# Kernel tuning notes

Measured on AMD Instinct MI355X. Metric: run time of the kernel, lower is better.

The kernel has to match this reference:

```python
import jax, jax.numpy as jnp
import numpy as np

DIM_PROBLEM = 256
DIM_CONTEXT = 1024
DIM_HIDDEN = 4096
INIT = 0.01


def setup_inputs() -> dict:
    key = jax.random.key(0)
    ks = jax.random.split(key, 12)
    H, C = DIM_HIDDEN, DIM_CONTEXT
    inp = {
        "context": jax.random.normal(ks[0], (C,), dtype=jnp.float32),
        "u": jax.random.uniform(ks[1], (DIM_PROBLEM,), dtype=jnp.float32),
        "l1_w": jax.random.normal(ks[2], (1, C), dtype=jnp.float32) * INIT,
        "l1_b": jnp.zeros((1,), dtype=jnp.float32),
        "Wf_w": jax.random.normal(ks[3], (H, H + 1), dtype=jnp.float32) * INIT,
        "Wf_b": jnp.zeros((H,), dtype=jnp.float32),
        "Wi_w": jax.random.normal(ks[4], (H, H + 1), dtype=jnp.float32) * INIT,
        "Wi_b": jnp.zeros((H,), dtype=jnp.float32),
        "Wc_w": jax.random.normal(ks[5], (H, H + 1), dtype=jnp.float32) * INIT,
        "Wc_b": jnp.zeros((H,), dtype=jnp.float32),
        "Wo_w": jax.random.normal(ks[6], (1, H + 1), dtype=jnp.float32) * INIT,
        "Wo_b": jnp.zeros((1,), dtype=jnp.float32),
    }
    return inp


def reference(context, u, l1_w, l1_b, Wf_w, Wf_b, Wi_w, Wi_b, Wc_w, Wc_b, Wo_w, Wo_b):
    H = Wf_w.shape[0]
    x0 = l1_w @ context + l1_b                      # (1,)
    h0 = jnp.zeros((H,), dtype=context.dtype)       # T.Tensor(H) treated as zeros
    c0 = jnp.zeros((H,), dtype=context.dtype)
    logp0 = jnp.zeros((1,), dtype=context.dtype)

    def step(carry, u_t):
        h, c, x, logp = carry
        z = jnp.concatenate([h, x])                 # (H+1,)
        f = jax.nn.sigmoid(Wf_w @ z + Wf_b)         # (H,)
        i = jax.nn.sigmoid(Wi_w @ z + Wi_b)
        cc = jnp.tanh(Wc_w @ z + Wc_b)
        o = jax.nn.sigmoid(Wo_w @ z + Wo_b)         # (1,)
        c_new = f * c + i * cc
        h_new = o * jnp.tanh(c_new)                 # broadcast (1,)*(H,)
        # detached Bernoulli(o) sample via pre-drawn uniform noise
        s = (u_t < jax.lax.stop_gradient(o)).astype(x.dtype)  # (1,)
        # log p accumulated: log(p * o^s * (1-o)^(1-s)) = logp + s*log o + (1-s)*log(1-o)
        logp_new = logp + s * jnp.log(o) + (1.0 - s) * jnp.log(1.0 - o)
        return (h_new, c_new, s, logp_new), s

    (_, _, _, logp), sol = jax.lax.scan(step, (h0, c0, x0, logp0), u)
    solution = sol[:, None, :]                      # (dim_problem, 1, 1)
    return solution, logp
```

## Files before the change

kernel.cpp:

```cpp
#include <hip/hip_runtime.h>
#include <hip/hip_fp16.h>
#include <stdint.h>


#define HID    4096
#define CTX    1024
#define NSTEPS 256
#define NBLK   256
#define TPB    1024
#define WAVES  16
#define HROWS  16
#define GROWS  48
#define RPW    3
#define NCH    8

typedef _Float16 h2 __attribute__((ext_vector_type(2)));

__device__ __forceinline__ float fdot2f(uint32_t a, uint32_t b, float c) {
#if __has_builtin(__builtin_amdgcn_fdot2)
  return __builtin_amdgcn_fdot2(__builtin_bit_cast(h2, a),
                                __builtin_bit_cast(h2, b), c, false);
#else
  h2 x = __builtin_bit_cast(h2, a), y = __builtin_bit_cast(h2, b);
  return c + (float)x[0]*(float)y[0] + (float)x[1]*(float)y[1];
#endif
}
__device__ __forceinline__ uint32_t pkf16(float x, float y) {
  h2 v; v[0] = (_Float16)x; v[1] = (_Float16)y;
  return __builtin_bit_cast(uint32_t, v);
}
__device__ __forceinline__ uint4 cvt8(const float* p) {
  return make_uint4(pkf16(p[0],p[1]), pkf16(p[2],p[3]),
                    pkf16(p[4],p[5]), pkf16(p[6],p[7]));
}
__device__ __forceinline__ float dot4(float acc, uint4 a, uint4 b) {
  acc = fdot2f(a.x, b.x, acc); acc = fdot2f(a.y, b.y, acc);
  acc = fdot2f(a.z, b.z, acc); acc = fdot2f(a.w, b.w, acc);
  return acc;
}
__device__ __forceinline__ void agw(uint32_t &slot, uint32_t v) {
  asm volatile("v_accvgpr_write_b32 %0, %1" : "=a"(slot) : "v"(v));
}
__device__ __forceinline__ uint32_t agr(uint32_t slot) {
  uint32_t v;
  asm("v_accvgpr_read_b32 %0, %1" : "=v"(v) : "a"(slot));
  return v;
}
__device__ __forceinline__ void stT(uint64_t* p, uint32_t payload, uint32_t tag) {
  const uint64_t v = ((uint64_t)tag << 32) | (uint64_t)payload;
  __hip_atomic_store(p, v, __ATOMIC_RELAXED, __HIP_MEMORY_SCOPE_AGENT);
}
__device__ __forceinline__ uint64_t ldT(const uint64_t* p) {
  return __hip_atomic_load(p, __ATOMIC_RELAXED, __HIP_MEMORY_SCOPE_AGENT);
}

__global__ __launch_bounds__(TPB)
void lstm(const float* __restrict__ ctx, const float* __restrict__ u,
          const float* __restrict__ l1w, const float* __restrict__ l1b,
          const float* __restrict__ Wf,  const float* __restrict__ Wfb,
          const float* __restrict__ Wi,  const float* __restrict__ Wib,
          const float* __restrict__ Wc,  const float* __restrict__ Wcb,
          const float* __restrict__ Wow, const float* __restrict__ Wob,
          uint64_t* __restrict__ hh0, uint64_t* __restrict__ hh1,
          uint64_t* __restrict__ part0, uint64_t* __restrict__ part1,
          float* __restrict__ out)
{
  __shared__ uint4 wlds[WAVES][HID/8];
  __shared__ uint4 zsh4[HID/8];
  __shared__ float red[WAVES];
  __shared__ float pre[GROWS];
  __shared__ float cst[HROWS];
  __shared__ float bias[GROWS];
  __shared__ float wx[GROWS];
  __shared__ float x0sh, osh, ssh;

  const int tid  = threadIdx.x;
  const int b    = blockIdx.x;
  const int wv   = tid >> 6;
  const int lane = tid & 63;

  uint32_t* z32 = (uint32_t*)zsh4;
  for (int i = tid; i < HID/2; i += TPB) z32[i] = 0u;
  if (tid < HROWS) cst[tid] = 0.f;
  if (tid < GROWS) {
    int g = tid / HROWS, j = tid % HROWS;
    const float* bw = (g==0 ? Wfb : (g==1 ? Wib : Wcb));
    const float* gw = (g==0 ? Wf  : (g==1 ? Wi  : Wc ));
    bias[tid] = bw[b*HROWS + j];
    wx[tid]   = gw[(size_t)(b*HROWS + j)*4097 + 4096];
  }

  const float wolocal = (tid < HROWS) ? Wow[b*HROWS + tid] : 0.f;
  const float woxw = Wow[HID];
  const float wob0 = Wob[0];

  uint32_t wreg[64];
  {
    const int fl0 = wv*RPW;
    const int g0 = (fl0+0)/HROWS, j0 = (fl0+0)%HROWS;
    const int g1 = (fl0+1)/HROWS, j1 = (fl0+1)%HROWS;
    const int g2 = (fl0+2)/HROWS, j2 = (fl0+2)%HROWS;
    const float* r0 = (g0==0?Wf:(g0==1?Wi:Wc)) + (size_t)(b*HROWS+j0)*4097;
    const float* r1 = (g1==0?Wf:(g1==1?Wi:Wc)) + (size_t)(b*HROWS+j1)*4097;
    const float* r2 = (g2==0?Wf:(g2==1?Wi:Wc)) + (size_t)(b*HROWS+j2)*4097;
    #pragma unroll
    for (int c = 0; c < NCH; ++c) {
      const int col = c*512 + lane*8;
      const uint4 va = cvt8(r0 + col);
      agw(wreg[c*8+0], va.x); agw(wreg[c*8+1], va.y);
      agw(wreg[c*8+2], va.z); agw(wreg[c*8+3], va.w);
      const uint4 vb = cvt8(r1 + col);
      agw(wreg[c*8+4], vb.x); agw(wreg[c*8+5], vb.y);
      agw(wreg[c*8+6], vb.z); agw(wreg[c*8+7], vb.w);
      wlds[wv][c*64 + lane] = cvt8(r2 + col);
    }
  }

  {
    float p = l1w[tid] * ctx[tid];
    #pragma unroll
    for (int off = 32; off; off >>= 1) p += __shfl_down(p, off, 64);
    __syncthreads();
    if (lane == 0) red[wv] = p;
    __syncthreads();
    if (tid == 0) {
      float ssum = 0.f;
      for (int w = 0; w < WAVES; ++w) ssum += red[w];
      x0sh = ssum + l1b[0];
    }
    __syncthreads();
  }
  float xcur = x0sh;
  float logp = 0.f;
  float ut = u[0];

  for (int t = 0; t < NSTEPS; ++t) {
    const uint64_t* prd = (t & 1) ? part0 : part1;
    uint64_t pv0 = 0, pv1 = 0, pv2 = 0, pv3 = 0;
    if (wv == 0 && t > 0) {
      pv0 = ldT(&prd[lane*4+0]); pv1 = ldT(&prd[lane*4+1]);
      pv2 = ldT(&prd[lane*4+2]); pv3 = ldT(&prd[lane*4+3]);
    }

    float a0 = 0.f, a1 = 0.f, a2 = 0.f;
    #pragma unroll
    for (int c = 0; c < NCH; ++c) {
      const uint4 zz = zsh4[c*64 + lane];
      const uint4 wl = wlds[wv][c*64 + lane];
      a0 = fdot2f(agr(wreg[c*8+0]), zz.x, a0);
      a0 = fdot2f(agr(wreg[c*8+1]), zz.y, a0);
      a0 = fdot2f(agr(wreg[c*8+2]), zz.z, a0);
      a0 = fdot2f(agr(wreg[c*8+3]), zz.w, a0);
      a1 = fdot2f(agr(wreg[c*8+4]), zz.x, a1);
      a1 = fdot2f(agr(wreg[c*8+5]), zz.y, a1);
      a1 = fdot2f(agr(wreg[c*8+6]), zz.z, a1);
      a1 = fdot2f(agr(wreg[c*8+7]), zz.w, a1);
      a2 = dot4(a2, wl, zz);
    }
    #pragma unroll
    for (int off = 32; off; off >>= 1) {
      a0 += __shfl_down(a0, off, 64);
      a1 += __shfl_down(a1, off, 64);
      a2 += __shfl_down(a2, off, 64);
    }

    if (wv == 0) {
      float ps = 0.f;
      if (t > 0) {
        const uint32_t tg = (uint32_t)t;
        while ((uint32_t)(pv0 >> 32) != tg) { __builtin_amdgcn_s_sleep(1); pv0 = ldT(&prd[lane*4+0]); }
        while ((uint32_t)(pv1 >> 32) != tg) { __builtin_amdgcn_s_sleep(1); pv1 = ldT(&prd[lane*4+1]); }
        while ((uint32_t)(pv2 >> 32) != tg) { __builtin_amdgcn_s_sleep(1); pv2 = ldT(&prd[lane*4+2]); }
        while ((uint32_t)(pv3 >> 32) != tg) { __builtin_amdgcn_s_sleep(1); pv3 = ldT(&prd[lane*4+3]); }
        const float q0 = __uint_as_float((uint32_t)pv0);
        const float q1 = __uint_as_float((uint32_t)pv1);
        const float q2 = __uint_as_float((uint32_t)pv2);
        const float q3 = __uint_as_float((uint32_t)pv3);
        ps = ((q0 + q1) + q2) + q3;
      }
      #pragma unroll
      for (int off = 32; off; off >>= 1) ps += __shfl_down(ps, off, 64);
      if (lane == 0) {
        const float opre = ps + woxw*xcur + wob0;
        const float o = 1.f / (1.f + expf(-opre));
        osh = o;
        ssh = (ut < o) ? 1.f : 0.f;
      }
    }
    if (lane == 0) {
      const int fl = wv*RPW;
      pre[fl+0] = a0 + wx[fl+0]*xcur + bias[fl+0];
      pre[fl+1] = a1 + wx[fl+1]*xcur + bias[fl+1];
      pre[fl+2] = a2 + wx[fl+2]*xcur + bias[fl+2];
    }
    __syncthreads();

    const float o = osh;
    const float s = ssh;
    uint64_t* hwH = (t & 1) ? hh1 : hh0;
    uint64_t* pwF = (t & 1) ? part1 : part0;
    float hv = 0.f;
    if (tid < HROWS) {
      const float ff = 1.f / (1.f + expf(-pre[tid]));
      const float ii = 1.f / (1.f + expf(-pre[HROWS+tid]));
      const float cc = tanhf(pre[2*HROWS+tid]);
      const float cn = ff*cst[tid] + ii*cc;
      cst[tid] = cn;
      hv = o * tanhf(cn);
    }
    if (tid < 64) {
      float pp = wolocal * hv;
      #pragma unroll
      for (int off = 8; off; off >>= 1) pp += __shfl_down(pp, off, 64);
      const float he = __shfl(hv, 2*(tid&7),   64);
      const float ho = __shfl(hv, 2*(tid&7)+1, 64);
      if (tid < 8) stT(&hwH[b*8 + tid], pkf16(he, ho), (uint32_t)(t+1));
      if (tid == 0) stT(&pwF[b], __float_as_uint(pp), (uint32_t)(t+1));
    }
    if (b == 0 && tid == 0) {
      logp += (s != 0.f) ? logf(o) : logf(1.f - o);
      out[t] = s;
    }
    xcur = s;

    if (t + 1 < NSTEPS) {
      const uint64_t* hr2 = (t & 1) ? hh1 : hh0;
      const uint32_t tg = (uint32_t)(t+1);
      uint64_t v0 = ldT(&hr2[tid]);
      uint64_t v1 = ldT(&hr2[tid + TPB]);
      while ((uint32_t)(v0 >> 32) != tg) {
        __builtin_amdgcn_s_sleep(1); v0 = ldT(&hr2[tid]);
      }
      while ((uint32_t)(v1 >> 32) != tg) {
        __builtin_amdgcn_s_sleep(1); v1 = ldT(&hr2[tid + TPB]);
      }
      z32[tid]       = (uint32_t)v0;
      z32[tid + TPB] = (uint32_t)v1;
      ut = u[t+1];
      __syncthreads();
    }
  }
  if (b == 0 && tid == 0) out[NSTEPS] = logp;
}

extern "C" void kernel_launch(void* const* d_in, const int* in_sizes, int n_in,
                              void* d_out, int out_size, void* d_ws, size_t ws_size,
                              hipStream_t stream) {
  const float* ctx = (const float*)d_in[0];
  const float* u   = (const float*)d_in[1];
  const float* l1w = (const float*)d_in[2];
  const float* l1b = (const float*)d_in[3];
  const float* Wf  = (const float*)d_in[4];
  const float* Wfb = (const float*)d_in[5];
  const float* Wi  = (const float*)d_in[6];
  const float* Wib = (const float*)d_in[7];
  const float* Wc  = (const float*)d_in[8];
  const float* Wcb = (const float*)d_in[9];
  const float* Wow = (const float*)d_in[10];
  const float* Wob = (const float*)d_in[11];
  float* out = (float*)d_out;

  char* ws = (char*)d_ws;
  uint64_t* part0 = (uint64_t*)(ws + 4096);
  uint64_t* part1 = (uint64_t*)(ws + 8192);
  uint64_t* hh0   = (uint64_t*)(ws + 12288);
  uint64_t* hh1   = (uint64_t*)(ws + 12288 + 16384);
  (void)hipMemsetAsync(ws + 4096, 0, 40960, stream);

  lstm<<<NBLK, TPB, 0, stream>>>(ctx,u,l1w,l1b,Wf,Wfb,Wi,Wib,Wc,Wcb,Wow,Wob,
                                 hh0,hh1,part0,part1,out);
}
```

Measured before the change: 1.030 ms.

## Compute forget/input gate matvecs with MFMA 16x16x32 f16 and LDS cross-wave reduction

The forget and input gate rows of each block move from per-lane fdot2 chains onto v_mfma_f32_16x16x32_f16. Each wave covers a 256-wide K slice for all 16 rows, and the z vector is broadcast as the B operand. Per-wave partial sums go to LDS and are summed by the first 16 threads, which replaces the two cross-lane shuffle reductions per wave. The candidate gate keeps the fdot2 path, now one row per wave. The MFMA does 16x redundant columns, and the serial 16-way LDS sum adds latency on the per-step critical path.

```diff
diff --git a/kernel.cpp b/kernel.cpp
--- a/kernel.cpp
+++ b/kernel.cpp
@@ -11,10 +11,11 @@
 #define WAVES  16
 #define HROWS  16
 #define GROWS  48
-#define RPW    3
 #define NCH    8
 
 typedef _Float16 h2 __attribute__((ext_vector_type(2)));
+typedef uint32_t u32x4v __attribute__((ext_vector_type(4)));
+typedef float    f32x4v __attribute__((ext_vector_type(4)));
 
 __device__ __forceinline__ float fdot2f(uint32_t a, uint32_t b, float c) {
 #if __has_builtin(__builtin_amdgcn_fdot2)
@@ -38,13 +39,12 @@
   acc = fdot2f(a.z, b.z, acc); acc = fdot2f(a.w, b.w, acc);
   return acc;
 }
-__device__ __forceinline__ void agw(uint32_t &slot, uint32_t v) {
-  asm volatile("v_accvgpr_write_b32 %0, %1" : "=a"(slot) : "v"(v));
-}
-__device__ __forceinline__ uint32_t agr(uint32_t slot) {
-  uint32_t v;
-  asm("v_accvgpr_read_b32 %0, %1" : "=v"(v) : "a"(slot));
-  return v;
+__device__ __forceinline__ void pinA(u32x4v &v) {
+  asm volatile("" : "+a"(v));
+}
+__device__ __forceinline__ f32x4v mfma16(const u32x4v a, const u32x4v b, f32x4v c) {
+  asm("v_mfma_f32_16x16x32_f16 %0, %1, %2, %0" : "+a"(c) : "a"(a), "v"(b));
+  return c;
 }
 __device__ __forceinline__ void stT(uint64_t* p, uint32_t payload, uint32_t tag) {
   const uint64_t v = ((uint64_t)tag << 32) | (uint64_t)payload;
@@ -68,7 +68,9 @@
   __shared__ uint4 wlds[WAVES][HID/8];
   __shared__ uint4 zsh4[HID/8];
   __shared__ float red[WAVES];
-  __shared__ float pre[GROWS];
+  __shared__ float partF[16][17];
+  __shared__ float partI[16][17];
+  __shared__ float pre_c[HROWS];
   __shared__ float cst[HROWS];
   __shared__ float bias[GROWS];
   __shared__ float wx[GROWS];
@@ -94,26 +96,23 @@
   const float woxw = Wow[HID];
   const float wob0 = Wob[0];
 
-  uint32_t wreg[64];
+  u32x4v ffr[8], ifr[8];
   {
-    const int fl0 = wv*RPW;
-    const int g0 = (fl0+0)/HROWS, j0 = (fl0+0)%HROWS;
-    const int g1 = (fl0+1)/HROWS, j1 = (fl0+1)%HROWS;
-    const int g2 = (fl0+2)/HROWS, j2 = (fl0+2)%HROWS;
-    const float* r0 = (g0==0?Wf:(g0==1?Wi:Wc)) + (size_t)(b*HROWS+j0)*4097;
-    const float* r1 = (g1==0?Wf:(g1==1?Wi:Wc)) + (size_t)(b*HROWS+j1)*4097;
-    const float* r2 = (g2==0?Wf:(g2==1?Wi:Wc)) + (size_t)(b*HROWS+j2)*4097;
-    #pragma unroll
-    for (int c = 0; c < NCH; ++c) {
-      const int col = c*512 + lane*8;
-      const uint4 va = cvt8(r0 + col);
-      agw(wreg[c*8+0], va.x); agw(wreg[c*8+1], va.y);
-      agw(wreg[c*8+2], va.z); agw(wreg[c*8+3], va.w);
-      const uint4 vb = cvt8(r1 + col);
-      agw(wreg[c*8+4], vb.x); agw(wreg[c*8+5], vb.y);
-      agw(wreg[c*8+6], vb.z); agw(wreg[c*8+7], vb.w);
-      wlds[wv][c*64 + lane] = cvt8(r2 + col);
-    }
+    const int arow  = b*HROWS + (lane & 15);
+    const int kbase = wv*256 + (lane >> 4)*8;
+    const float* rfA = Wf + (size_t)arow*4097 + kbase;
+    const float* riA = Wi + (size_t)arow*4097 + kbase;
+    #pragma unroll
+    for (int mi = 0; mi < 8; ++mi) {
+      ffr[mi] = __builtin_bit_cast(u32x4v, cvt8(rfA + mi*32)); pinA(ffr[mi]);
+      ifr[mi] = __builtin_bit_cast(u32x4v, cvt8(riA + mi*32)); pinA(ifr[mi]);
+    }
+  }
+  {
+    const float* rc = Wc + (size_t)(b*HROWS + wv)*4097;
+    #pragma unroll
+    for (int c = 0; c < NCH; ++c)
+      wlds[wv][c*64 + lane] = cvt8(rc + c*512 + lane*8);
   }
 
   {
@@ -142,27 +141,28 @@
       pv2 = ldT(&prd[lane*4+2]); pv3 = ldT(&prd[lane*4+3]);
     }
 
-    float a0 = 0.f, a1 = 0.f, a2 = 0.f;
+    f32x4v accf = {0.f, 0.f, 0.f, 0.f};
+    f32x4v acci = {0.f, 0.f, 0.f, 0.f};
+    {
+      const int zb2 = wv*128 + (lane >> 4)*4;
+      #pragma unroll
+      for (int mi = 0; mi < 8; ++mi) {
+        const u32x4v bz =
+            __builtin_bit_cast(u32x4v, *(const uint4*)&z32[zb2 + mi*16]);
+        accf = mfma16(ffr[mi], bz, accf);
+        acci = mfma16(ifr[mi], bz, acci);
+      }
+    }
+
+    float a2 = 0.f;
     #pragma unroll
     for (int c = 0; c < NCH; ++c) {
       const uint4 zz = zsh4[c*64 + lane];
       const uint4 wl = wlds[wv][c*64 + lane];
-      a0 = fdot2f(agr(wreg[c*8+0]), zz.x, a0);
-      a0 = fdot2f(agr(wreg[c*8+1]), zz.y, a0);
-      a0 = fdot2f(agr(wreg[c*8+2]), zz.z, a0);
-      a0 = fdot2f(agr(wreg[c*8+3]), zz.w, a0);
-      a1 = fdot2f(agr(wreg[c*8+4]), zz.x, a1);
-      a1 = fdot2f(agr(wreg[c*8+5]), zz.y, a1);
-      a1 = fdot2f(agr(wreg[c*8+6]), zz.z, a1);
-      a1 = fdot2f(agr(wreg[c*8+7]), zz.w, a1);
       a2 = dot4(a2, wl, zz);
     }
     #pragma unroll
-    for (int off = 32; off; off >>= 1) {
-      a0 += __shfl_down(a0, off, 64);
-      a1 += __shfl_down(a1, off, 64);
-      a2 += __shfl_down(a2, off, 64);
-    }
+    for (int off = 32; off; off >>= 1) a2 += __shfl_down(a2, off, 64);
 
     if (wv == 0) {
       float ps = 0.f;
@@ -187,11 +187,15 @@
         ssh = (ut < o) ? 1.f : 0.f;
       }
     }
-    if (lane == 0) {
-      const int fl = wv*RPW;
-      pre[fl+0] = a0 + wx[fl+0]*xcur + bias[fl+0];
-      pre[fl+1] = a1 + wx[fl+1]*xcur + bias[fl+1];
-      pre[fl+2] = a2 + wx[fl+2]*xcur + bias[fl+2];
+    if (lane == 0)
+      pre_c[wv] = a2 + wx[32+wv]*xcur + bias[32+wv];
+    if ((lane & 15) == 0) {
+      const int g = lane >> 4;
+      #pragma unroll
+      for (int r = 0; r < 4; ++r) {
+        partF[g*4+r][wv] = accf[r];
+        partI[g*4+r][wv] = acci[r];
+      }
     }
     __syncthreads();
 
@@ -201,9 +205,14 @@
     uint64_t* pwF = (t & 1) ? part1 : part0;
     float hv = 0.f;
     if (tid < HROWS) {
-      const float ff = 1.f / (1.f + expf(-pre[tid]));
-      const float ii = 1.f / (1.f + expf(-pre[HROWS+tid]));
-      const float cc = tanhf(pre[2*HROWS+tid]);
+      float sf = 0.f, si = 0.f;
+      #pragma unroll
+      for (int w = 0; w < WAVES; ++w) { sf += partF[tid][w]; si += partI[tid][w]; }
+      const float pf = sf + wx[tid]*xcur + bias[tid];
+      const float pi = si + wx[16+tid]*xcur + bias[16+tid];
+      const float ff = 1.f / (1.f + expf(-pf));
+      const float ii = 1.f / (1.f + expf(-pi));
+      const float cc = tanhf(pre_c[tid]);
       const float cn = ff*cst[tid] + ii*cc;
       cst[tid] = cn;
       hv = o * tanhf(cn);
```

After: 1.616 ms. 1.57x slower.
